# Optimization experiments

Measured on AMD Instinct MI355X. Metric: run time of the kernel, lower is better.

Reference implementation:

```python
import jax, jax.numpy as jnp
import numpy as np

N_NODES = 50000
N_EDGES = 800000
IN_F = 128
OUT_F = 256


def setup_inputs() -> dict:
    key = jax.random.key(0)
    k1, k2, k3, k4, k5, k6 = jax.random.split(key, 6)
    x = jax.random.normal(k1, (N_NODES, IN_F), dtype=jnp.float32)
    edge_row = jax.random.randint(k2, (N_EDGES,), 0, N_NODES, dtype=jnp.int32)
    edge_col = jax.random.randint(k3, (N_EDGES,), 0, N_NODES, dtype=jnp.int32)
    edge_val = jax.random.uniform(k4, (N_EDGES,), dtype=jnp.float32)
    weight = jax.random.normal(k5, (IN_F, OUT_F), dtype=jnp.float32) * (1.0 / np.sqrt(OUT_F))
    b = jax.random.normal(k6, (OUT_F,), dtype=jnp.float32) * 0.01
    return {"x": x, "edge_row": edge_row, "edge_col": edge_col,
            "edge_val": edge_val, "weight": weight, "b": b}


def reference(x, edge_row, edge_col, edge_val, weight, b):
    # spmm: agg[i] = sum_{e: row[e]==i} val[e] * x[col[e]]
    msgs = edge_val[:, None] * x[edge_col]              # [E, in_f]
    agg = jax.ops.segment_sum(msgs, edge_row, num_segments=x.shape[0])  # [N, in_f]
    # dense transform + bias
    return agg @ weight + b                              # [N, out_f]
```

## Files before the change

### kernel.cpp

```cpp
#include <hip/hip_runtime.h>
#include <hip/hip_bf16.h>

#define N_NODES 50000
#define N_EDGES 800000
#define IN_F    128
#define OUT_F   256
#define CAP     96

typedef __attribute__((ext_vector_type(8))) short  short8;
typedef __attribute__((ext_vector_type(4))) float  f32x4;

static __device__ __forceinline__ unsigned short f2bf(float f) {
    __hip_bfloat16 h = __float2bfloat16(f);
    return *reinterpret_cast<unsigned short*>(&h);
}


__global__ __launch_bounds__(256)
void convert_x(const float* __restrict__ x, unsigned short* __restrict__ xb, int n8) {
    const int i = blockIdx.x * blockDim.x + threadIdx.x;
    if (i >= n8) return;
    const float4* xp = reinterpret_cast<const float4*>(x) + (size_t)i * 2;
    const float4 a = xp[0], b = xp[1];
    uint4 o;
    o.x = (unsigned)f2bf(a.x) | ((unsigned)f2bf(a.y) << 16);
    o.y = (unsigned)f2bf(a.z) | ((unsigned)f2bf(a.w) << 16);
    o.z = (unsigned)f2bf(b.x) | ((unsigned)f2bf(b.y) << 16);
    o.w = (unsigned)f2bf(b.z) | ((unsigned)f2bf(b.w) << 16);
    reinterpret_cast<uint4*>(xb)[i] = o;
}

__global__ __launch_bounds__(256)
void convert_w(const float* __restrict__ W, unsigned short* __restrict__ Wt) {
    const int n  = blockIdx.x * 16 + (threadIdx.x & 15);
    const int kc = threadIdx.x >> 4;
    unsigned q[4];
#pragma unroll
    for (int j = 0; j < 4; ++j) {
        const int k = kc * 8 + j * 2;
        const unsigned short u0 = f2bf(W[(size_t)k * OUT_F + n]);
        const unsigned short u1 = f2bf(W[(size_t)(k + 1) * OUT_F + n]);
        q[j] = (unsigned)u0 | ((unsigned)u1 << 16);
    }
    *reinterpret_cast<uint4*>(Wt + (size_t)n * IN_F + kc * 8) =
        make_uint4(q[0], q[1], q[2], q[3]);
}

__global__ __launch_bounds__(256)
void bucket_fill(const int* __restrict__ row, const int* __restrict__ col,
                 const float* __restrict__ val, int* __restrict__ cnt,
                 unsigned long long* __restrict__ recs, int E) {
    int e = blockIdx.x * blockDim.x + threadIdx.x;
    if (e >= E) return;
    const int r = row[e];
    const int slot = atomicAdd(&cnt[r], 1);
    if (slot < CAP) {
        const unsigned long long rec =
            ((unsigned long long)__float_as_uint(val[e]) << 32) | (unsigned)col[e];
        recs[(size_t)r * CAP + slot] = rec;
    }
}

__global__ __launch_bounds__(256)
void gcn_fused(const unsigned short* __restrict__ xb,
               const int* __restrict__ cnt,
               const unsigned long long* __restrict__ recs,
               const unsigned short* __restrict__ Wt,
               const float* __restrict__ bias,
               float* __restrict__ out, int M) {
    __shared__ unsigned short sA[16][IN_F];

    const int tid  = threadIdx.x;
    const int wv   = tid >> 6;
    const int lane = tid & 63;
    const int es   = lane >> 3;
    const int fg   = lane & 7;
    const int base = blockIdx.x * 16;

    for (int s = 0; s < 4; ++s) {
        const int nl   = wv * 4 + s;
        const int node = base + nl;

        float acc[16];
#pragma unroll
        for (int i = 0; i < 16; ++i) acc[i] = 0.f;

        int d = 0;
        if (node < M) d = min(cnt[node], CAP);
        const size_t st = (size_t)node * CAP;

        for (int j0 = 0; j0 < d; j0 += 8) {
            const int  idx = j0 + es;
            const bool ok  = (idx < d);
            const unsigned long long rec = recs[st + (ok ? idx : 0)];
            const int   c = (int)(unsigned)(rec & 0xffffffffull);
            const float v = ok ? __uint_as_float((unsigned)(rec >> 32)) : 0.f;

            const uint4* xp = reinterpret_cast<const uint4*>(
                xb + (size_t)c * IN_F + fg * 16);
            const uint4 a = xp[0], b = xp[1];
            const unsigned w[8] = {a.x, a.y, a.z, a.w, b.x, b.y, b.z, b.w};
#pragma unroll
            for (int j = 0; j < 8; ++j) {
                acc[2 * j]     += v * __uint_as_float(w[j] << 16);
                acc[2 * j + 1] += v * __uint_as_float(w[j] & 0xffff0000u);
            }
        }

#pragma unroll
        for (int i = 0; i < 16; ++i) {
            acc[i] += __shfl_xor(acc[i], 8);
            acc[i] += __shfl_xor(acc[i], 16);
            acc[i] += __shfl_xor(acc[i], 32);
        }

        if (es == 0) {
            unsigned q[8];
#pragma unroll
            for (int j = 0; j < 8; ++j)
                q[j] = (unsigned)f2bf(acc[2 * j]) |
                       ((unsigned)f2bf(acc[2 * j + 1]) << 16);
            unsigned short* sp = &sA[nl][fg * 16];
            reinterpret_cast<uint4*>(sp)[0] = make_uint4(q[0], q[1], q[2], q[3]);
            reinterpret_cast<uint4*>(sp)[1] = make_uint4(q[4], q[5], q[6], q[7]);
        }
    }
    __syncthreads();

    const int lr = lane & 15;
    const int lg = lane >> 4;

    short8 af[4];
#pragma unroll
    for (int kk = 0; kk < 4; ++kk)
        af[kk] = *reinterpret_cast<const short8*>(&sA[lr][kk * 32 + lg * 8]);

    const int crow = base + lr;
    float* orow = out + (size_t)crow * OUT_F;

#pragma unroll
    for (int t = 0; t < 4; ++t) {
        const int nt   = wv * 4 + t;
        const int wcol = nt * 16 + lr;
        short8 wf[4];
#pragma unroll
        for (int kk = 0; kk < 4; ++kk)
            wf[kk] = *reinterpret_cast<const short8*>(
                Wt + (size_t)wcol * IN_F + kk * 32 + lg * 8);

        f32x4 acc = (f32x4){0.f, 0.f, 0.f, 0.f};
#pragma unroll
        for (int kk = 0; kk < 4; ++kk)
            acc = __builtin_amdgcn_mfma_f32_16x16x32_bf16(
                wf[kk], af[kk], acc, 0, 0, 0);

        const float4 bv = *reinterpret_cast<const float4*>(bias + nt * 16 + lg * 4);
        if (crow < M) {
            const float4 o = make_float4(acc[0] + bv.x, acc[1] + bv.y,
                                         acc[2] + bv.z, acc[3] + bv.w);
            *reinterpret_cast<float4*>(orow + nt * 16 + lg * 4) = o;
        }
    }
}

extern "C" void kernel_launch(void* const* d_in, const int* in_sizes, int n_in,
                              void* d_out, int out_size, void* d_ws, size_t ws_size,
                              hipStream_t stream) {
    const float* x        = (const float*)d_in[0];
    const int*   edge_row = (const int*)  d_in[1];
    const int*   edge_col = (const int*)  d_in[2];
    const float* edge_val = (const float*)d_in[3];
    const float* weight   = (const float*)d_in[4];
    const float* bias     = (const float*)d_in[5];
    float* out = (float*)d_out;

    char* w = (char*)d_ws;
    unsigned short* xb = (unsigned short*)w;
    unsigned long long* recs = (unsigned long long*)(w + 12800000);
    unsigned short* Wt = (unsigned short*)(w + 51200000);
    int* cnt = (int*)(w + 51265536);

    hipMemsetAsync(cnt, 0, (size_t)N_NODES * sizeof(int), stream);

    convert_x<<<(N_NODES * IN_F / 8 + 255) / 256, 256, 0, stream>>>(
        x, xb, N_NODES * IN_F / 8);
    convert_w<<<16, 256, 0, stream>>>(weight, Wt);

    bucket_fill<<<(N_EDGES + 255) / 256, 256, 0, stream>>>(
        edge_row, edge_col, edge_val, cnt, recs, N_EDGES);

    gcn_fused<<<(N_NODES + 15) / 16, 256, 0, stream>>>(
        xb, cnt, recs, Wt, bias, out, N_NODES);
}
```

Before: 201.9 us.

## Merge prep kernels, unroll edge gather by two, swizzle LDS tile

Folds the x conversion, weight conversion and edge bucketing into one launch with block-range dispatch, which removes two kernel launch gaps and lets the independent work overlap. Bucket records are now written with nontemporal stores. The aggregation loop handles two edge batches per iteration so more gather loads are in flight at once. The shared-memory A tile gets an XOR swizzle to cut bank conflicts on the MFMA fragment reads. The risks are higher register pressure in the gather loop and the prep block counts being hardcoded to the problem sizes.

```diff
diff --git a/kernel.cpp b/kernel.cpp
--- a/kernel.cpp
+++ b/kernel.cpp
@@ -16,48 +16,53 @@
 }
 
 
+#define CX_BLOCKS 3125
+#define BF_BLOCKS 3125
+#define CW_BLOCKS 16
+
 __global__ __launch_bounds__(256)
-void convert_x(const float* __restrict__ x, unsigned short* __restrict__ xb, int n8) {
-    const int i = blockIdx.x * blockDim.x + threadIdx.x;
-    if (i >= n8) return;
-    const float4* xp = reinterpret_cast<const float4*>(x) + (size_t)i * 2;
-    const float4 a = xp[0], b = xp[1];
-    uint4 o;
-    o.x = (unsigned)f2bf(a.x) | ((unsigned)f2bf(a.y) << 16);
-    o.y = (unsigned)f2bf(a.z) | ((unsigned)f2bf(a.w) << 16);
-    o.z = (unsigned)f2bf(b.x) | ((unsigned)f2bf(b.y) << 16);
-    o.w = (unsigned)f2bf(b.z) | ((unsigned)f2bf(b.w) << 16);
-    reinterpret_cast<uint4*>(xb)[i] = o;
-}
-
-__global__ __launch_bounds__(256)
-void convert_w(const float* __restrict__ W, unsigned short* __restrict__ Wt) {
-    const int n  = blockIdx.x * 16 + (threadIdx.x & 15);
-    const int kc = threadIdx.x >> 4;
-    unsigned q[4];
-#pragma unroll
-    for (int j = 0; j < 4; ++j) {
-        const int k = kc * 8 + j * 2;
-        const unsigned short u0 = f2bf(W[(size_t)k * OUT_F + n]);
-        const unsigned short u1 = f2bf(W[(size_t)(k + 1) * OUT_F + n]);
-        q[j] = (unsigned)u0 | ((unsigned)u1 << 16);
-    }
-    *reinterpret_cast<uint4*>(Wt + (size_t)n * IN_F + kc * 8) =
-        make_uint4(q[0], q[1], q[2], q[3]);
-}
-
-__global__ __launch_bounds__(256)
-void bucket_fill(const int* __restrict__ row, const int* __restrict__ col,
-                 const float* __restrict__ val, int* __restrict__ cnt,
-                 unsigned long long* __restrict__ recs, int E) {
-    int e = blockIdx.x * blockDim.x + threadIdx.x;
-    if (e >= E) return;
-    const int r = row[e];
-    const int slot = atomicAdd(&cnt[r], 1);
-    if (slot < CAP) {
-        const unsigned long long rec =
-            ((unsigned long long)__float_as_uint(val[e]) << 32) | (unsigned)col[e];
-        recs[(size_t)r * CAP + slot] = rec;
+void prep(const float* __restrict__ x, unsigned short* __restrict__ xb,
+          const float* __restrict__ W, unsigned short* __restrict__ Wt,
+          const int* __restrict__ row, const int* __restrict__ col,
+          const float* __restrict__ val,
+          int* __restrict__ cnt, unsigned long long* __restrict__ recs) {
+    const int b   = blockIdx.x;
+    const int tid = threadIdx.x;
+
+    if (b < CX_BLOCKS) {
+        const int i = b * 256 + tid;
+        const float4* xp = reinterpret_cast<const float4*>(x) + (size_t)i * 2;
+        const float4 a = xp[0], c = xp[1];
+        uint4 o;
+        o.x = (unsigned)f2bf(a.x) | ((unsigned)f2bf(a.y) << 16);
+        o.y = (unsigned)f2bf(a.z) | ((unsigned)f2bf(a.w) << 16);
+        o.z = (unsigned)f2bf(c.x) | ((unsigned)f2bf(c.y) << 16);
+        o.w = (unsigned)f2bf(c.z) | ((unsigned)f2bf(c.w) << 16);
+        reinterpret_cast<uint4*>(xb)[i] = o;
+    } else if (b < CX_BLOCKS + BF_BLOCKS) {
+        const int e = (b - CX_BLOCKS) * 256 + tid;
+        const int r = row[e];
+        const int slot = atomicAdd(&cnt[r], 1);
+        if (slot < CAP) {
+            const unsigned long long rec =
+                ((unsigned long long)__float_as_uint(val[e]) << 32) |
+                (unsigned)col[e];
+            __builtin_nontemporal_store(rec, &recs[(size_t)r * CAP + slot]);
+        }
+    } else {
+        const int bb = b - (CX_BLOCKS + BF_BLOCKS);
+        const int n  = bb * 16 + (tid & 15);
+        const int kc = tid >> 4;
+        unsigned q[4];
+#pragma unroll
+        for (int j = 0; j < 4; ++j) {
+            const int k = kc * 8 + j * 2;
+            const unsigned short u0 = f2bf(W[(size_t)k * OUT_F + n]);
+            const unsigned short u1 = f2bf(W[(size_t)(k + 1) * OUT_F + n]);
+            q[j] = (unsigned)u0 | ((unsigned)u1 << 16);
+        }
+        *reinterpret_cast<uint4*>(Wt + (size_t)n * IN_F + kc * 8) =
+            make_uint4(q[0], q[1], q[2], q[3]);
     }
 }
 
@@ -68,7 +73,7 @@
                const unsigned short* __restrict__ Wt,
                const float* __restrict__ bias,
                float* __restrict__ out, int M) {
-    __shared__ unsigned short sA[16][IN_F];
+    __shared__ uint4 sA[16 * 16];
 
     const int tid  = threadIdx.x;
     const int wv   = tid >> 6;
@@ -87,23 +92,38 @@
 
         int d = 0;
         if (node < M) d = min(cnt[node], CAP);
-        const size_t st = (size_t)node * CAP;
-
-        for (int j0 = 0; j0 < d; j0 += 8) {
-            const int  idx = j0 + es;
-            const bool ok  = (idx < d);
-            const unsigned long long rec = recs[st + (ok ? idx : 0)];
-            const int   c = (int)(unsigned)(rec & 0xffffffffull);
-            const float v = ok ? __uint_as_float((unsigned)(rec >> 32)) : 0.f;
-
-            const uint4* xp = reinterpret_cast<const uint4*>(
-                xb + (size_t)c * IN_F + fg * 16);
-            const uint4 a = xp[0], b = xp[1];
-            const unsigned w[8] = {a.x, a.y, a.z, a.w, b.x, b.y, b.z, b.w};
+        const unsigned long long* bp = recs + (size_t)node * CAP;
+
+        for (int j0 = 0; j0 < d; j0 += 16) {
+            const int  i0  = j0 + es;
+            const int  i1  = j0 + 8 + es;
+            const bool ok0 = (i0 < d);
+            const bool ok1 = (i1 < d);
+            const unsigned long long r0 = bp[ok0 ? i0 : 0];
+            const unsigned long long r1 = bp[ok1 ? i1 : 0];
+            const int   c0 = (int)(unsigned)(r0 & 0xffffffffull);
+            const int   c1 = (int)(unsigned)(r1 & 0xffffffffull);
+            const float v0 = ok0 ? __uint_as_float((unsigned)(r0 >> 32)) : 0.f;
+            const float v1 = ok1 ? __uint_as_float((unsigned)(r1 >> 32)) : 0.f;
+
+            const uint4* p0 = reinterpret_cast<const uint4*>(
+                xb + (size_t)c0 * IN_F + fg * 16);
+            const uint4* p1 = reinterpret_cast<const uint4*>(
+                xb + (size_t)c1 * IN_F + fg * 16);
+            const uint4 a0 = p0[0], b0 = p0[1];
+            const uint4 a1 = p1[0], b1 = p1[1];
+
+            const unsigned w0[8] = {a0.x, a0.y, a0.z, a0.w, b0.x, b0.y, b0.z, b0.w};
+            const unsigned w1[8] = {a1.x, a1.y, a1.z, a1.w, b1.x, b1.y, b1.z, b1.w};
 #pragma unroll
             for (int j = 0; j < 8; ++j) {
-                acc[2 * j]     += v * __uint_as_float(w[j] << 16);
-                acc[2 * j + 1] += v * __uint_as_float(w[j] & 0xffff0000u);
+                acc[2 * j]     += v0 * __uint_as_float(w0[j] << 16);
+                acc[2 * j + 1] += v0 * __uint_as_float(w0[j] & 0xffff0000u);
+            }
+#pragma unroll
+            for (int j = 0; j < 8; ++j) {
+                acc[2 * j]     += v1 * __uint_as_float(w1[j] << 16);
+                acc[2 * j + 1] += v1 * __uint_as_float(w1[j] & 0xffff0000u);
             }
         }
 
@@ -120,9 +140,8 @@
             for (int j = 0; j < 8; ++j)
                 q[j] = (unsigned)f2bf(acc[2 * j]) |
                        ((unsigned)f2bf(acc[2 * j + 1]) << 16);
-            unsigned short* sp = &sA[nl][fg * 16];
-            reinterpret_cast<uint4*>(sp)[0] = make_uint4(q[0], q[1], q[2], q[3]);
-            reinterpret_cast<uint4*>(sp)[1] = make_uint4(q[4], q[5], q[6], q[7]);
+            sA[nl * 16 + ((fg * 2)     ^ nl)] = make_uint4(q[0], q[1], q[2], q[3]);
+            sA[nl * 16 + ((fg * 2 + 1) ^ nl)] = make_uint4(q[4], q[5], q[6], q[7]);
         }
     }
     __syncthreads();
@@ -132,8 +151,10 @@
 
     short8 af[4];
 #pragma unroll
-    for (int kk = 0; kk < 4; ++kk)
-        af[kk] = *reinterpret_cast<const short8*>(&sA[lr][kk * 32 + lg * 8]);
+    for (int kk = 0; kk < 4; ++kk) {
+        const uint4 u = sA[lr * 16 + ((kk * 4 + lg) ^ lr)];
+        af[kk] = *reinterpret_cast<const short8*>(&u);
+    }
 
     const int crow = base + lr;
     float* orow = out + (size_t)crow * OUT_F;
@@ -182,12 +203,8 @@
 
     hipMemsetAsync(cnt, 0, (size_t)N_NODES * sizeof(int), stream);
 
-    convert_x<<<(N_NODES * IN_F / 8 + 255) / 256, 256, 0, stream>>>(
-        x, xb, N_NODES * IN_F / 8);
-    convert_w<<<16, 256, 0, stream>>>(weight, Wt);
-
-    bucket_fill<<<(N_EDGES + 255) / 256, 256, 0, stream>>>(
-        edge_row, edge_col, edge_val, cnt, recs, N_EDGES);
+    prep<<<CX_BLOCKS + BF_BLOCKS + CW_BLOCKS, 256, 0, stream>>>(
+        x, xb, weight, Wt, edge_row, edge_col, edge_val, cnt, recs);
 
     gcn_fused<<<(N_NODES + 15) / 16, 256, 0, stream>>>(
         xb, cnt, recs, Wt, bias, out, N_NODES);
```

After: 221.9 us. 9.9% more time.
